# Performance work log

Hardware: AMD Instinct MI355X
Metric: run time of the kernel (lower is better)

Reference implementation:

```python
import jax, jax.numpy as jnp
import numpy as np

B, S, E, H = 8, 512, 768, 12
EPS = 1e-5  # torch LayerNorm default

def setup_inputs() -> dict:
    key = jax.random.key(0)
    ks = jax.random.split(key, 6)
    s = 1.0 / np.sqrt(E)
    return {
        "x": jax.random.normal(ks[0], (B, S, E), jnp.float32),
        "atten_pad_mask": jax.random.randint(ks[1], (B, 1, S), 0, 2, jnp.int32),
        # per-head shared q/k/v projection weights, stacked: [H, E_in, E_out]
        "Wh": jax.random.normal(ks[2], (H, E, E), jnp.float32) * s,
        "bh": jax.random.normal(ks[3], (H, E), jnp.float32) * s,
        # output projection: [H*E, E]
        "Wo": jax.random.normal(ks[4], (H * E, E), jnp.float32) * (1.0 / np.sqrt(H * E)),
        "bo": jnp.zeros((E,), jnp.float32),
        "gamma": jnp.ones((E,), jnp.float32),
        "beta": jnp.zeros((E,), jnp.float32),
    }

def reference(x, atten_pad_mask, Wh, bh, Wo, bo, gamma, beta):
    # Each head applies ONE shared linear to q=k=v=x (faithful to SelfAttention).
    p = jnp.einsum('bse,heo->bhso', x, Wh) + bh[None, :, None, :]  # [B,H,S,E]
    scores = jnp.einsum('bhqe,bhke->bhqk', p, p) / np.sqrt(E)      # [B,H,S,S]
    # masked_fill(mask == 1, -inf); mask [B,1,S] -> broadcast [B,1,1,S]
    scores = jnp.where(atten_pad_mask[:, None, :, :] == 1, -jnp.inf, scores)
    attn = jax.nn.softmax(scores, axis=-1)
    o = jnp.einsum('bhqk,bhke->bhqe', attn, p)                     # [B,H,S,E]
    cat = o.transpose(0, 2, 1, 3).reshape(B, S, H * E)             # concat heads
    y = cat @ Wo + bo                                              # [B,S,E]
    mu = jnp.mean(y, axis=-1, keepdims=True)
    var = jnp.var(y, axis=-1, keepdims=True)
    return (y - mu) / jnp.sqrt(var + EPS) * gamma + beta
```

## Files before the change

kernel.cpp:

```cpp
#include <hip/hip_runtime.h>
#include <hip/hip_bf16.h>
#include <math.h>

#define B_ 8
#define S_ 512
#define E_ 768
#define H_ 12
#define HE_ (H_ * E_)
#define KSPLIT 6
#define KCHUNK (HE_ / KSPLIT)

typedef __attribute__((ext_vector_type(4))) short bf16x4;
typedef __attribute__((ext_vector_type(8))) short bf16x8;
typedef __attribute__((ext_vector_type(16))) float f32x16;

__device__ inline void gload_lds16(const void* g, void* l) {
  __builtin_amdgcn_global_load_lds(
      (const __attribute__((address_space(1))) unsigned int*)g,
      (__attribute__((address_space(3))) unsigned int*)l, 16, 0, 0);
}

__device__ inline float bf2f(short u) {
  union { float f; unsigned int i; } c;
  c.i = ((unsigned int)(unsigned short)u) << 16;
  return c.f;
}
__device__ inline short f2bf(float f) {
  __hip_bfloat16 h = __float2bfloat16(f);
  return *reinterpret_cast<short*>(&h);
}

__global__ __launch_bounds__(256) void cvt_v(const float* __restrict__ in,
                                             short* __restrict__ out) {
  const long i = ((long)blockIdx.x * 256 + threadIdx.x) * 4;
  float4 v = *reinterpret_cast<const float4*>(in + i);
  bf16x4 o;
  o[0] = f2bf(v.x); o[1] = f2bf(v.y); o[2] = f2bf(v.z); o[3] = f2bf(v.w);
  *reinterpret_cast<bf16x4*>(out + i) = o;
}

__global__ __launch_bounds__(512) void mask_scan(const int* __restrict__ mask,
                                                 int* __restrict__ idx,
                                                 int* __restrict__ cntp) {
  const int b = blockIdx.x;
  const int t = threadIdx.x;
  const int wave = t >> 6, lane = t & 63;
  const bool keep = (mask[b * S_ + t] == 0);
  unsigned long long bal = __ballot(keep);
  const int wprefix = __popcll(bal & ((1ull << lane) - 1ull));
  __shared__ int wt[8];
  if (lane == 0) wt[wave] = __popcll(bal);
  idx[b * S_ + t] = 0;
  __syncthreads();
  int off = 0, total = 0;
#pragma unroll
  for (int i = 0; i < 8; ++i) {
    off += (i < wave) ? wt[i] : 0;
    total += wt[i];
  }
  if (keep) idx[b * S_ + off + wprefix] = t;
  if (t == 0) {
    cntp[2 * b] = total;
    int pad = (total + 63) & ~63;
    cntp[2 * b + 1] = pad > S_ ? S_ : pad;
  }
}

template <typename T, int VW>
__global__ __launch_bounds__(256) void transpose_v(const T* __restrict__ in, long inz,
                                                   short* __restrict__ out, long outz,
                                                   int R, int C) {
  __shared__ float t[64][65];
  in += (long)blockIdx.z * inz;
  out += (long)blockIdx.z * outz;
  const int bc = blockIdx.x * 64, br = blockIdx.y * 64;
  const int tid = threadIdx.x;
  constexpr int CPR = 64 / VW;
  constexpr int NP1 = 64 * CPR / 256;
#pragma unroll
  for (int ps = 0; ps < NP1; ++ps) {
    int q = tid + ps * 256;
    int r = q / CPR, c0 = (q % CPR) * VW;
    const T* src = in + (long)(br + r) * C + bc + c0;
    if constexpr (VW == 4) {
      float4 v = *reinterpret_cast<const float4*>(src);
      t[r][c0] = v.x; t[r][c0 + 1] = v.y; t[r][c0 + 2] = v.z; t[r][c0 + 3] = v.w;
    } else {
      bf16x8 v = *reinterpret_cast<const bf16x8*>(src);
#pragma unroll
      for (int j = 0; j < 8; ++j) t[r][c0 + j] = bf2f(v[j]);
    }
  }
  __syncthreads();
#pragma unroll
  for (int ps = 0; ps < 2; ++ps) {
    int q = tid + ps * 256;
    int e = q >> 3, s0 = (q & 7) * 8;
    bf16x8 o;
#pragma unroll
    for (int j = 0; j < 8; ++j) o[j] = f2bf(t[s0 + j][e]);
    *reinterpret_cast<bf16x8*>(out + (long)(bc + e) * R + br + s0) = o;
  }
}

__global__ __launch_bounds__(256) void transpose_gather(const short* __restrict__ p,
                                                        const int* __restrict__ gidx,
                                                        const int* __restrict__ cntp,
                                                        short* __restrict__ out) {
  const int z = blockIdx.z, b = z / H_;
  const int br = blockIdx.y * 64;
  if (br >= cntp[2 * b + 1]) return;
  __shared__ float t[64][65];
  const short* in = p + (long)z * S_ * E_;
  short* o = out + (long)z * S_ * E_;
  const int bc = blockIdx.x * 64;
  const int tid = threadIdx.x;
#pragma unroll
  for (int ps = 0; ps < 2; ++ps) {
    int q = tid + ps * 256;
    int r = q >> 3, c0 = (q & 7) * 8;
    int srow = gidx[b * S_ + br + r];
    bf16x8 v = *reinterpret_cast<const bf16x8*>(in + (long)srow * E_ + bc + c0);
#pragma unroll
    for (int j = 0; j < 8; ++j) t[r][c0 + j] = bf2f(v[j]);
  }
  __syncthreads();
#pragma unroll
  for (int ps = 0; ps < 2; ++ps) {
    int q = tid + ps * 256;
    int e = q >> 3, s0 = (q & 7) * 8;
    bf16x8 o8;
#pragma unroll
    for (int j = 0; j < 8; ++j) o8[j] = f2bf(t[s0 + j][e]);
    *reinterpret_cast<bf16x8*>(o + (long)(bc + e) * S_ + br + s0) = o8;
  }
}

template <bool OUT_BF16, bool ADD_BIAS, bool GATHER_B, bool K_FROM_CNT>
__global__ __launch_bounds__(256) void gemm_bt(
    const __hip_bfloat16* __restrict__ A, long As1, long As2, int lda,
    const __hip_bfloat16* __restrict__ BT, long Bs1, long Bs2, int ldb,
    void* __restrict__ Cv, long Cs1, long Cs2, int ldc,
    const float* __restrict__ bias, long biasS2, int zmod, int K, float scale,
    int nx, int ny, const int* __restrict__ gidx, const int* __restrict__ cntp) {
  constexpr int BM = 128, BN = 128, BK = 64;
  __shared__ __align__(16) __hip_bfloat16 sA[BM * BK];
  __shared__ __align__(16) __hip_bfloat16 sB[BN * BK];
  const int nwg = gridDim.x;
  const int cpx = nwg >> 3;
  const int id = blockIdx.x;
  const int w = (id & 7) * cpx + (id >> 3);
  const int bz = w / (nx * ny);
  const int rem = w - bz * nx * ny;
  const int by = rem / nx;
  const int bx = rem - by * nx;

  const int tid = threadIdx.x;
  const int wave = tid >> 6, lane = tid & 63;
  const int r32 = lane & 31, g2 = lane >> 5;
  const int zb = bz / zmod, zh = bz % zmod;
  const int bm = by * BM, bn = bx * BN;
  if (GATHER_B && bn >= cntp[2 * zb + 1]) return;
  int Keff = K;
  if (K_FROM_CNT) Keff = cntp[2 * zb + 1];
  A += (long)zb * As1 + (long)zh * As2;
  BT += (long)zb * Bs1 + (long)zh * Bs2;
  const int wm = (wave >> 1) * 64, wn = (wave & 1) * 64;
  const int swz = (r32 & 7) << 3;
  f32x16 acc[2][2] = {};
  const int e0 = tid * 8;

  int colp[4], rowp[4], growB[4];
#pragma unroll
  for (int p = 0; p < 4; ++p) {
    int ee = p * 2048 + e0;
    int row = ee >> 6;
    rowp[p] = row;
    colp[p] = (ee & 63) ^ ((row & 7) << 3);
    growB[p] = GATHER_B ? gidx[zb * S_ + bn + row] : (bn + row);
  }

  for (int k0 = 0; k0 < Keff; k0 += BK) {
#pragma unroll
    for (int p = 0; p < 4; ++p) {
      int ee = p * 2048 + e0;
      gload_lds16(A + (long)(bm + rowp[p]) * lda + (k0 + colp[p]), (char*)sA + ee * 2);
      gload_lds16(BT + (long)growB[p] * ldb + (k0 + colp[p]), (char*)sB + ee * 2);
    }
    __syncthreads();
#pragma unroll
    for (int ks = 0; ks < 4; ++ks) {
      bf16x8 aw[2], bw[2];
#pragma unroll
      for (int ti = 0; ti < 2; ++ti) {
        int row = wm + ti * 32 + r32;
        int c = (ks * 16 + g2 * 8) ^ swz;
        aw[ti] = *(const bf16x8*)(const void*)(sA + row * BK + c);
      }
#pragma unroll
      for (int tj = 0; tj < 2; ++tj) {
        int row = wn + tj * 32 + r32;
        int c = (ks * 16 + g2 * 8) ^ swz;
        bw[tj] = *(const bf16x8*)(const void*)(sB + row * BK + c);
      }
#pragma unroll
      for (int ti = 0; ti < 2; ++ti)
#pragma unroll
        for (int tj = 0; tj < 2; ++tj)
          acc[ti][tj] =
              __builtin_amdgcn_mfma_f32_32x32x16_bf16(aw[ti], bw[tj], acc[ti][tj], 0, 0, 0);
    }
    __syncthreads();
  }

  float* Cf = (float*)Cv;
  __hip_bfloat16* Cb = (__hip_bfloat16*)Cv;
  const long cbase = (long)zb * Cs1 + (long)zh * Cs2;
#pragma unroll
  for (int ti = 0; ti < 2; ++ti)
#pragma unroll
    for (int tj = 0; tj < 2; ++tj) {
      const int colv = bn + wn + tj * 32 + r32;
      const float bv = ADD_BIAS ? bias[(long)zh * biasS2 + colv] : 0.0f;
#pragma unroll
      for (int r = 0; r < 16; ++r) {
        int rowv = bm + wm + ti * 32 + (r & 3) + 8 * (r >> 2) + 4 * g2;
        float v = acc[ti][tj][r] * scale + bv;
        long off = cbase + (long)rowv * ldc + colv;
        if (OUT_BF16)
          Cb[off] = __float2bfloat16(v);
        else
          Cf[off] = v;
      }
    }
}

__global__ __launch_bounds__(256) void softmax_v(__hip_bfloat16* __restrict__ scores,
                                                 const int* __restrict__ cntp) {
  const int wave = threadIdx.x >> 6, lane = threadIdx.x & 63;
  const long row = (long)blockIdx.x * 4 + wave;
  const int b = (int)(row / ((long)H_ * S_));
  const int cnt = cntp[2 * b];
  short* sp = (short*)scores + row * S_ + lane * 8;
  bf16x8 sv = *reinterpret_cast<const bf16x8*>(sp);
  const int j0 = lane * 8;
  float v[8];
#pragma unroll
  for (int j = 0; j < 8; ++j) v[j] = (j0 + j < cnt) ? bf2f(sv[j]) : -INFINITY;
  float mx = v[0];
#pragma unroll
  for (int j = 1; j < 8; ++j) mx = fmaxf(mx, v[j]);
#pragma unroll
  for (int o = 32; o; o >>= 1) mx = fmaxf(mx, __shfl_xor(mx, o));
  float e[8], s = 0.0f;
#pragma unroll
  for (int j = 0; j < 8; ++j) {
    e[j] = expf(v[j] - mx);
    s += e[j];
  }
#pragma unroll
  for (int o = 32; o; o >>= 1) s += __shfl_xor(s, o);
  const float inv = 1.0f / s;
  bf16x8 o8;
#pragma unroll
  for (int j = 0; j < 8; ++j) o8[j] = f2bf(e[j] * inv);
  *reinterpret_cast<bf16x8*>(sp) = o8;
}

__global__ __launch_bounds__(192) void ln_v(const __hip_bfloat16* __restrict__ yp,
                                            const float* __restrict__ bo,
                                            const float* __restrict__ gamma,
                                            const float* __restrict__ beta,
                                            float* __restrict__ out) {
  const long nY = (long)B_ * S_ * E_;
  const long base = (long)blockIdx.x * E_;
  const int t = threadIdx.x;
  const int c0 = t * 4;
  float a[4];
  {
    float4 bv = *reinterpret_cast<const float4*>(bo + c0);
    a[0] = bv.x; a[1] = bv.y; a[2] = bv.z; a[3] = bv.w;
  }
#pragma unroll
  for (int k = 0; k < KSPLIT; ++k) {
    bf16x4 v = *reinterpret_cast<const bf16x4*>((const short*)yp + k * nY + base + c0);
#pragma unroll
    for (int j = 0; j < 4; ++j) a[j] += bf2f(v[j]);
  }
  float s = a[0] + a[1] + a[2] + a[3];
  float ss = a[0] * a[0] + a[1] * a[1] + a[2] * a[2] + a[3] * a[3];
#pragma unroll
  for (int o = 32; o; o >>= 1) {
    s += __shfl_xor(s, o);
    ss += __shfl_xor(ss, o);
  }
  __shared__ float r1[3], r2[3];
  const int wave = t >> 6, lane = t & 63;
  if (lane == 0) { r1[wave] = s; r2[wave] = ss; }
  __syncthreads();
  s = r1[0] + r1[1] + r1[2];
  ss = r2[0] + r2[1] + r2[2];
  const float mu = s * (1.0f / E_);
  const float var = ss * (1.0f / E_) - mu * mu;
  const float rstd = rsqrtf(var + 1e-5f);
  float4 g = *reinterpret_cast<const float4*>(gamma + c0);
  float4 bt = *reinterpret_cast<const float4*>(beta + c0);
  float4 o4;
  o4.x = (a[0] - mu) * rstd * g.x + bt.x;
  o4.y = (a[1] - mu) * rstd * g.y + bt.y;
  o4.z = (a[2] - mu) * rstd * g.z + bt.z;
  o4.w = (a[3] - mu) * rstd * g.w + bt.w;
  *reinterpret_cast<float4*>(out + base + c0) = o4;
}

extern "C" void kernel_launch(void* const* d_in, const int* in_sizes, int n_in,
                              void* d_out, int out_size, void* d_ws, size_t ws_size,
                              hipStream_t stream) {
  const float* x = (const float*)d_in[0];
  const int* mask = (const int*)d_in[1];
  const float* Wh = (const float*)d_in[2];
  const float* bh = (const float*)d_in[3];
  const float* Wo = (const float*)d_in[4];
  const float* bo = (const float*)d_in[5];
  const float* gamma = (const float*)d_in[6];
  const float* beta = (const float*)d_in[7];
  float* out = (float*)d_out;

  const size_t nX = (size_t)B_ * S_ * E_;
  const size_t nWh = (size_t)H_ * E_ * E_;
  const size_t nP = (size_t)B_ * H_ * S_ * E_;
  const size_t nSc = (size_t)B_ * H_ * S_ * S_;
  char* base = (char*)d_ws;
  __hip_bfloat16* p = (__hip_bfloat16*)base;
  __hip_bfloat16* cat = p;
  char* RB = base + nP * 2;
  __hip_bfloat16* pcT = (__hip_bfloat16*)RB;
  __hip_bfloat16* ypart = (__hip_bfloat16*)RB;
  char* RC = RB + nP * 2;
  __hip_bfloat16* xb = (__hip_bfloat16*)RC;
  __hip_bfloat16* WhT = (__hip_bfloat16*)(RC + nX * 2);
  __hip_bfloat16* scores = (__hip_bfloat16*)RC;
  char* RD = RC + nSc * 2;
  __hip_bfloat16* WoT = (__hip_bfloat16*)RD;
  int* idx = (int*)(RD + nWh * 2);
  int* cntp = idx + B_ * S_;

  dim3 t256(256);
  const float inv_sqrtE = 1.0f / sqrtf((float)E_);

  mask_scan<<<dim3(B_), dim3(512), 0, stream>>>(mask, idx, cntp);
  cvt_v<<<dim3(nX / 1024), t256, 0, stream>>>(x, (short*)xb);
  transpose_v<float, 4><<<dim3(12, 12, 12), t256, 0, stream>>>(
      Wh, (long)E_ * E_, (short*)WhT, (long)E_ * E_, E_, E_);
  transpose_v<float, 4><<<dim3(12, 144, 1), t256, 0, stream>>>(
      Wo, 0, (short*)WoT, 0, HE_, E_);
  gemm_bt<true, true, false, false><<<dim3(6 * 4 * 96), t256, 0, stream>>>(
      xb, (long)S_ * E_, 0, E_, WhT, 0, (long)E_ * E_, E_, p, (long)H_ * S_ * E_,
      (long)S_ * E_, E_, bh, E_, H_, E_, 1.0f, 6, 4, nullptr, nullptr);
  gemm_bt<true, false, true, false><<<dim3(4 * 4 * 96), t256, 0, stream>>>(
      p, (long)H_ * S_ * E_, (long)S_ * E_, E_, p, (long)H_ * S_ * E_, (long)S_ * E_, E_,
      scores, (long)H_ * S_ * S_, (long)S_ * S_, S_, nullptr, 0, H_, E_, inv_sqrtE, 4, 4,
      idx, cntp);
  softmax_v<<<dim3(12288), t256, 0, stream>>>(scores, cntp);
  transpose_gather<<<dim3(12, 8, 96), t256, 0, stream>>>((const short*)p, idx, cntp,
                                                         (short*)pcT);
  gemm_bt<true, false, false, true><<<dim3(6 * 4 * 96), t256, 0, stream>>>(
      scores, (long)H_ * S_ * S_, (long)S_ * S_, S_, pcT, (long)H_ * E_ * S_,
      (long)E_ * S_, S_, cat, (long)S_ * HE_, (long)E_, HE_, nullptr, 0, H_, S_, 1.0f,
      6, 4, nullptr, cntp);
  gemm_bt<true, false, false, false><<<dim3(6 * 32 * KSPLIT), t256, 0, stream>>>(
      cat, 0, KCHUNK, HE_, WoT, 0, KCHUNK, HE_, ypart, 0, (long)B_ * S_ * E_, E_,
      nullptr, 0, KSPLIT, KCHUNK, 1.0f, 6, 32, nullptr, nullptr);
  ln_v<<<dim3(B_ * S_), dim3(192), 0, stream>>>(ypart, bo, gamma, beta, out);
}
```

Before: 278.8 us.

## Double-buffer LDS tiles in bf16 GEMM and raise output-projection K split

Converts the shared GEMM main loop to a two-stage LDS double buffer. The global-to-LDS load of the next K tile is issued before computing on the current tile, with one barrier per iteration instead of two, so memory latency overlaps MFMA work. It also raises KSPLIT from 6 to 8, giving the output projection more, smaller K chunks. The cost is doubled LDS use per block (64KB), which may lower occupancy, and more partial sums to reduce.

```diff
diff --git a/kernel.cpp b/kernel.cpp
--- a/kernel.cpp
+++ b/kernel.cpp
@@ -7,7 +7,7 @@
 #define E_ 768
 #define H_ 12
 #define HE_ (H_ * E_)
-#define KSPLIT 6
+#define KSPLIT 8
 #define KCHUNK (HE_ / KSPLIT)
 
 typedef __attribute__((ext_vector_type(4))) short bf16x4;
@@ -144,8 +144,8 @@
     const float* __restrict__ bias, long biasS2, int zmod, int K, float scale,
     int nx, int ny, const int* __restrict__ gidx, const int* __restrict__ cntp) {
   constexpr int BM = 128, BN = 128, BK = 64;
-  __shared__ __align__(16) __hip_bfloat16 sA[BM * BK];
-  __shared__ __align__(16) __hip_bfloat16 sB[BN * BK];
+  __shared__ __align__(16) __hip_bfloat16 sA[2][BM * BK];
+  __shared__ __align__(16) __hip_bfloat16 sB[2][BN * BK];
   const int nwg = gridDim.x;
   const int cpx = nwg >> 3;
   const int id = blockIdx.x;
@@ -180,14 +180,29 @@
     growB[p] = GATHER_B ? gidx[zb * S_ + bn + row] : (bn + row);
   }
 
-  for (int k0 = 0; k0 < Keff; k0 += BK) {
+  auto stage = [&](int t, int buf) {
+    const int k0 = t * BK;
 #pragma unroll
     for (int p = 0; p < 4; ++p) {
       int ee = p * 2048 + e0;
-      gload_lds16(A + (long)(bm + rowp[p]) * lda + (k0 + colp[p]), (char*)sA + ee * 2);
-      gload_lds16(BT + (long)growB[p] * ldb + (k0 + colp[p]), (char*)sB + ee * 2);
-    }
-    __syncthreads();
+      gload_lds16(A + (long)(bm + rowp[p]) * lda + (k0 + colp[p]),
+                  (char*)(sA[buf]) + ee * 2);
+      gload_lds16(BT + (long)growB[p] * ldb + (k0 + colp[p]),
+                  (char*)(sB[buf]) + ee * 2);
+    }
+  };
+
+  const int NT = Keff / BK;
+  stage(0, 0);
+  asm volatile("s_waitcnt vmcnt(0)" ::: "memory");
+  __builtin_amdgcn_sched_barrier(0);
+  __builtin_amdgcn_s_barrier();
+
+  int cur = 0;
+  for (int t = 0; t < NT; ++t) {
+    if (t + 1 < NT) stage(t + 1, cur ^ 1);
+    const __hip_bfloat16* pA = sA[cur];
+    const __hip_bfloat16* pB = sB[cur];
 #pragma unroll
     for (int ks = 0; ks < 4; ++ks) {
       bf16x8 aw[2], bw[2];
@@ -195,13 +210,13 @@
       for (int ti = 0; ti < 2; ++ti) {
         int row = wm + ti * 32 + r32;
         int c = (ks * 16 + g2 * 8) ^ swz;
-        aw[ti] = *(const bf16x8*)(const void*)(sA + row * BK + c);
+        aw[ti] = *(const bf16x8*)(const void*)(pA + row * BK + c);
       }
 #pragma unroll
       for (int tj = 0; tj < 2; ++tj) {
         int row = wn + tj * 32 + r32;
         int c = (ks * 16 + g2 * 8) ^ swz;
-        bw[tj] = *(const bf16x8*)(const void*)(sB + row * BK + c);
+        bw[tj] = *(const bf16x8*)(const void*)(pB + row * BK + c);
       }
 #pragma unroll
       for (int ti = 0; ti < 2; ++ti)
@@ -210,7 +225,12 @@
           acc[ti][tj] =
               __builtin_amdgcn_mfma_f32_32x32x16_bf16(aw[ti], bw[tj], acc[ti][tj], 0, 0, 0);
     }
-    __syncthreads();
+    if (t + 1 < NT) {
+      asm volatile("s_waitcnt vmcnt(0)" ::: "memory");
+      __builtin_amdgcn_sched_barrier(0);
+      __builtin_amdgcn_s_barrier();
+      cur ^= 1;
+    }
   }
 
   float* Cf = (float*)Cv;
```

New measurement: 316.0 us. 1.13x slower.
